# Performance work log

Measured on AMD Instinct MI355X. Metric: run time of the kernel, lower is better.

The kernel has to match this reference:

```python
import jax, jax.numpy as jnp
import numpy as np

N_HEADS = 8
D_HEAD = 64
SCALE = D_HEAD ** -0.5


def setup_inputs() -> dict:
    key = jax.random.key(0)
    k1, k2, k3 = jax.random.split(key, 3)
    B, H, W, C = 16, 32, 32, 512
    ft = jax.random.normal(k1, (B, H, W, C), dtype=jnp.float32)
    # Dense layers: to_qkv -> n_heads*n_dim_heads*3 = 1536 units, to_out -> n_channels
    w_qkv = jax.random.normal(k2, (C, N_HEADS * D_HEAD * 3), dtype=jnp.float32) * (C ** -0.5)
    b_qkv = jnp.zeros((N_HEADS * D_HEAD * 3,), dtype=jnp.float32)
    w_out = jax.random.normal(k3, (N_HEADS * D_HEAD, C), dtype=jnp.float32) * ((N_HEADS * D_HEAD) ** -0.5)
    b_out = jnp.zeros((C,), dtype=jnp.float32)
    return {"ft": ft, "w_qkv": w_qkv, "b_qkv": b_qkv, "w_out": w_out, "b_out": b_out}


def reference(ft, w_qkv, b_qkv, w_out, b_out):
    B, H, W, C = ft.shape
    N = H * W
    x = ft.reshape(B, N, C)                       # b (h w) c
    qkv = x @ w_qkv + b_qkv                       # b n (heads * 3*d_head)
    qkv = qkv.reshape(B, N, N_HEADS, 3 * D_HEAD)  # 'b x (h d) -> b x h d'
    q, k, v = jnp.split(qkv, 3, axis=-1)          # each: b n heads d_head
    attn = jnp.einsum('bxhd,byhd->bxyh', q, k) * SCALE
    attn = jax.nn.softmax(attn, axis=2)           # softmax over key axis y
    res = jnp.einsum('bxyh,byhd->bxhd', attn, v)  # b x h d
    res = res.reshape(B, N, N_HEADS * D_HEAD)     # 'b x h d -> b x (h d)'
    res = res @ w_out + b_out
    res = res + x                                 # residual with pre-qkv flattened input
    return res.reshape(B, H, W, C)
```

## Files before the change

kernel.cpp:

```cpp
#include <hip/hip_runtime.h>
#include <hip/hip_bf16.h>

using u16 = unsigned short;
using u32 = unsigned int;
typedef __attribute__((ext_vector_type(8))) short short8;
typedef __attribute__((ext_vector_type(4))) float f32x4;

#define MFMA16(A, B, C) __builtin_amdgcn_mfma_f32_16x16x32_bf16((A), (B), (C), 0, 0, 0)

__device__ __forceinline__ u16 f2bf(float f) {
  union { float f; u32 i; } v; v.f = f;
  u32 x = v.i;
  return (u16)((x + 0x7fffu + ((x >> 16) & 1u)) >> 16);
}
__device__ __forceinline__ u32 pkbf(float a, float b) {
  union { __hip_bfloat162 h; u32 u; } v;
  v.h = __float22bfloat162_rn(make_float2(a, b));
  return v.u;
}
__device__ __forceinline__ u32 cvtpk(float a, float b) {
  u32 r;
  asm("v_cvt_pk_bf16_f32 %0, %1, %2" : "=v"(r) : "v"(a), "v"(b));
  return r;
}
__device__ __forceinline__ void gl16(const u16* g, u16* l) {
  __builtin_amdgcn_global_load_lds(
      (const __attribute__((address_space(1))) u32*)g,
      (__attribute__((address_space(3))) u32*)l, 16, 0, 0);
}

__global__ __launch_bounds__(256) void conv_x(const float* __restrict__ X,
                                              u16* __restrict__ Xbf) {
  const int i = (blockIdx.x * 256 + threadIdx.x) * 8;
  float4 a = *(const float4*)(X + i);
  float4 b = *(const float4*)(X + i + 4);
  uint4 o;
  o.x = pkbf(a.x, a.y); o.y = pkbf(a.z, a.w);
  o.z = pkbf(b.x, b.y); o.w = pkbf(b.z, b.w);
  *(uint4*)(Xbf + i) = o;
}

__global__ __launch_bounds__(256) void transpose_w(
    const float* __restrict__ Wq, const float* __restrict__ Wo,
    u16* __restrict__ Wqt, u16* __restrict__ Wot) {
  const int z = blockIdx.z;
  if (z == 1 && blockIdx.x >= 16) return;
  const float* src = z ? Wo : Wq;
  u16* dst = z ? Wot : Wqt;
  const int ncols = z ? 512 : 1536;
  __shared__ float tile[32][33];
  const int t = threadIdx.x;
  const int kt = blockIdx.y * 32, nt = blockIdx.x * 32;
  const int r = t >> 3, c4 = (t & 7) * 4;
  float4 v = *(const float4*)(src + (size_t)(kt + r) * ncols + nt + c4);
  tile[r][c4 + 0] = v.x; tile[r][c4 + 1] = v.y;
  tile[r][c4 + 2] = v.z; tile[r][c4 + 3] = v.w;
  __syncthreads();
  uint2 p = make_uint2(pkbf(tile[c4 + 0][r], tile[c4 + 1][r]),
                       pkbf(tile[c4 + 2][r], tile[c4 + 3][r]));
  *(uint2*)(dst + (size_t)(nt + r) * 512 + kt + c4) = p;
}

__global__ __launch_bounds__(512) void qkv_gemm(
    const u16* __restrict__ Xbf, const u16* __restrict__ Wt,
    const float* __restrict__ Bias,
    u16* __restrict__ Qp, u16* __restrict__ Kp, u16* __restrict__ Vt) {
  __shared__ u16 Xs[2][128][32];
  __shared__ u16 Ws[2][256][32];
  const int t = threadIdx.x;
  const int bm = blockIdx.y * 128, bn = blockIdx.x * 256;
  const int w = t >> 6, lane = t & 63, quad = lane >> 4, l16 = lane & 15;
  const int mtb = (w >> 2) * 64, ntb = (w & 3) * 64;
  const int rr = lane >> 2;
  const int gch = ((lane & 3) ^ ((lane >> 3) & 3)) * 8;
  const int sw = (quad ^ ((l16 >> 1) & 3)) * 8;

  const u16* xg0 = Xbf + (size_t)(bm + w * 16 + rr) * 512 + gch;
  const u16* wg0 = Wt + (size_t)(bn + w * 16 + rr) * 512 + gch;
  const u16* wg1 = wg0 + (size_t)128 * 512;
  u16* xl[2] = {&Xs[0][w * 16][0], &Xs[1][w * 16][0]};
  u16* wl[2] = {&Ws[0][w * 16][0], &Ws[1][w * 16][0]};

  f32x4 acc[4][4];
  const f32x4 z4 = {0.f, 0.f, 0.f, 0.f};
  #pragma unroll
  for (int mi = 0; mi < 4; mi++)
    #pragma unroll
    for (int ni = 0; ni < 4; ni++) acc[mi][ni] = z4;

  gl16(xg0, xl[0]);
  gl16(wg0, wl[0]); gl16(wg1, wl[0] + 4096);
  __syncthreads();

  for (int k0 = 0; k0 < 512; k0 += 32) {
    const int cur = (k0 >> 5) & 1;
    if (k0 < 480) {
      const int nxt = cur ^ 1, kn = k0 + 32;
      gl16(xg0 + kn, xl[nxt]);
      gl16(wg0 + kn, wl[nxt]); gl16(wg1 + kn, wl[nxt] + 4096);
    }
    short8 af[4], bf4[4];
    #pragma unroll
    for (int mi = 0; mi < 4; mi++)
      af[mi] = *(const short8*)&Xs[cur][mtb + mi * 16 + l16][sw];
    #pragma unroll
    for (int ni = 0; ni < 4; ni++)
      bf4[ni] = *(const short8*)&Ws[cur][ntb + ni * 16 + l16][sw];
    #pragma unroll
    for (int mi = 0; mi < 4; mi++)
      #pragma unroll
      for (int ni = 0; ni < 4; ni++)
        acc[mi][ni] = MFMA16(af[mi], bf4[ni], acc[mi][ni]);
    __syncthreads();
  }

  #pragma unroll
  for (int ni = 0; ni < 4; ni++) {
    const int g = bn + ntb + ni * 16;
    const int h = g / 192, rm = g % 192;
    const int type = rm >> 6, dbase = rm & 63;
    const float bias = Bias[g + l16];
    const float qsc = (type == 0) ? 0.125f * 1.44269504088896340736f : 1.0f;
    #pragma unroll
    for (int mi = 0; mi < 4; mi++) {
      const int row0 = bm + mtb + mi * 16 + quad * 4;
      const int b = row0 >> 10, n0 = row0 & 1023;
      const size_t bh = (size_t)(b * 8 + h) * 65536;
      if (type == 2) {
        uint2 p = make_uint2(pkbf(acc[mi][ni][0] + bias, acc[mi][ni][1] + bias),
                             pkbf(acc[mi][ni][2] + bias, acc[mi][ni][3] + bias));
        *(uint2*)(Vt + bh + (size_t)(dbase + l16) * 1024 + n0) = p;
      } else {
        u16* dst = (type ? Kp : Qp) + bh;
        #pragma unroll
        for (int r = 0; r < 4; r++)
          dst[(size_t)(n0 + r) * 64 + dbase + l16] =
              f2bf((acc[mi][ni][r] + bias) * qsc);
      }
    }
  }
}

__global__ __launch_bounds__(512, 8) void attn_mfma(
    const u16* __restrict__ Qp, const u16* __restrict__ Kp,
    const u16* __restrict__ Vt, u16* __restrict__ ATT) {
  __shared__ u16 Ks[2][64][64];
  __shared__ u16 Vs[2][64][64];
  const int t = threadIdx.x, w = t >> 6, lane = t & 63;
  const int quad = lane >> 4, l16 = lane & 15;
  const int bx = blockIdx.x;
  const int c = bx & 7, g = bx >> 3;
  const int qt = g & 7, u = g >> 3;
  const int bh_id = u * 8 + c;
  const int b = bh_id >> 3, h = bh_id & 7;
  const size_t bh = (size_t)bh_id * 65536;
  const u16* Qb = Qp + bh;
  const u16* Kb = Kp + bh;
  const u16* Vb = Vt + bh;
  const int q0 = qt * 128 + w * 16;

  const u16* kg = Kb + (size_t)(t >> 3) * 64 + ((t & 7) ^ ((t >> 3) & 7)) * 8;
  const u16* vg = Vb + (size_t)(t >> 3) * 1024 + ((t & 7) ^ ((t >> 3) & 7)) * 8;
  u16* ks0 = &Ks[0][0][0] + w * 512;
  u16* ks1 = &Ks[1][0][0] + w * 512;
  u16* vs0 = &Vs[0][0][0] + w * 512;
  u16* vs1 = &Vs[1][0][0] + w * 512;

  const int m7 = l16 & 7;
  const char* ksb = (const char*)&Ks[0][0][0];
  const char* vsb = (const char*)&Vs[0][0][0];
  const int kb0 = l16 * 128 + (quad ^ m7) * 16;
  const int kb1 = kb0 ^ 64;
  int vo[2];
  #pragma unroll
  for (int ks = 0; ks < 2; ks++)
    vo[ks] = l16 * 128 + ((4 * ks + quad) ^ m7) * 16;

  short8 qf[2];
  #pragma unroll
  for (int ks = 0; ks < 2; ks++)
    qf[ks] = *(const short8*)(Qb + (size_t)(q0 + l16) * 64 + ks * 32 + quad * 8);

  float l_ = 0.f;
  f32x4 Of[4];
  const f32x4 z4 = {0.f, 0.f, 0.f, 0.f};
  #pragma unroll
  for (int ni = 0; ni < 4; ni++) Of[ni] = z4;

  gl16(kg, ks0);
  gl16(vg, vs0);
  __syncthreads();

  for (int kt = 0; kt < 16; ++kt) {
    const int cur = kt & 1;
    if (kt < 15) {
      gl16(kg + (kt + 1) * 4096, cur ? ks0 : ks1);
      gl16(vg + (kt + 1) * 64,   cur ? vs0 : vs1);
    }
    const int co = cur << 13;

    u32 e[4], o[4];
    #pragma unroll
    for (int nt = 0; nt < 4; nt++) {
      short8 k0f = *(const short8*)(ksb + co + kb0 + nt * 2048);
      short8 k1f = *(const short8*)(ksb + co + kb1 + nt * 2048);
      f32x4 s = z4;
      s = MFMA16(k0f, qf[0], s);
      s = MFMA16(k1f, qf[1], s);
      float p0 = __builtin_amdgcn_exp2f(s[0]);
      float p1 = __builtin_amdgcn_exp2f(s[1]);
      float p2 = __builtin_amdgcn_exp2f(s[2]);
      float p3 = __builtin_amdgcn_exp2f(s[3]);
      l_ += (p0 + p1) + (p2 + p3);
      const u32 lo = cvtpk(p0, p1), hi = cvtpk(p2, p3);
      if (nt & 1) { o[(nt >> 1) * 2] = lo; o[(nt >> 1) * 2 + 1] = hi; }
      else        { e[(nt >> 1) * 2] = lo; e[(nt >> 1) * 2 + 1] = hi; }
    }
    #pragma unroll
    for (int i = 0; i < 4; i++) {
      auto t01 = __builtin_amdgcn_permlane32_swap(e[i], o[i], false, false);
      auto xy  = __builtin_amdgcn_permlane16_swap(t01[0], t01[1], false, false);
      e[i] = xy[0]; o[i] = xy[1];
    }
    #pragma unroll
    for (int ks = 0; ks < 2; ks++) {
      union { short8 v; u32 u[4]; } pa;
      pa.u[0] = e[2 * ks]; pa.u[1] = e[2 * ks + 1];
      pa.u[2] = o[2 * ks]; pa.u[3] = o[2 * ks + 1];
      #pragma unroll
      for (int ni = 0; ni < 4; ni++) {
        short8 vf = *(const short8*)(vsb + co + vo[ks] + ni * 2048);
        Of[ni] = MFMA16(pa.v, vf, Of[ni]);
      }
    }
    __syncthreads();
  }
  l_ += __shfl_xor(l_, 16);
  l_ += __shfl_xor(l_, 32);
  float lv[4];
  #pragma unroll
  for (int r = 0; r < 4; r++) lv[r] = __shfl(l_, quad * 4 + r);
  #pragma unroll
  for (int r = 0; r < 4; r++) {
    const float inv = 1.0f / lv[r];
    const int row = b * 1024 + q0 + quad * 4 + r;
    #pragma unroll
    for (int ni = 0; ni < 4; ni++)
      ATT[(size_t)row * 512 + h * 64 + ni * 16 + l16] = f2bf(Of[ni][r] * inv);
  }
}

__global__ __launch_bounds__(256) void out_proj(
    const u16* __restrict__ A, const u16* __restrict__ Wt,
    const float* __restrict__ Bias, const float* __restrict__ FT,
    float* __restrict__ OUT) {
  __shared__ u16 As[2][128][32];
  __shared__ u16 Ws[2][128][32];
  const int t = threadIdx.x;
  const int bm = blockIdx.y * 128, bn = blockIdx.x * 128;
  const int w = t >> 6, lane = t & 63, quad = lane >> 4, l16 = lane & 15;
  const int mtb = (w >> 1) * 64, ntb = (w & 1) * 64;
  const int rr = lane >> 2;
  const int gch = ((lane & 3) ^ ((lane >> 3) & 3)) * 8;
  const int sw = (quad ^ ((l16 >> 1) & 3)) * 8;

  const u16* ag0 = A + (size_t)(bm + w * 16 + rr) * 512 + gch;
  const u16* ag1 = ag0 + (size_t)64 * 512;
  const u16* wg0 = Wt + (size_t)(bn + w * 16 + rr) * 512 + gch;
  const u16* wg1 = wg0 + (size_t)64 * 512;
  u16* al0[2] = {&As[0][w * 16][0], &As[1][w * 16][0]};
  u16* wl0[2] = {&Ws[0][w * 16][0], &Ws[1][w * 16][0]};

  f32x4 acc[4][4];
  const f32x4 z4 = {0.f, 0.f, 0.f, 0.f};
  #pragma unroll
  for (int mi = 0; mi < 4; mi++)
    #pragma unroll
    for (int ni = 0; ni < 4; ni++) acc[mi][ni] = z4;

  gl16(ag0, al0[0]); gl16(ag1, al0[0] + 2048);
  gl16(wg0, wl0[0]); gl16(wg1, wl0[0] + 2048);
  __syncthreads();

  for (int k0 = 0; k0 < 512; k0 += 32) {
    const int cur = (k0 >> 5) & 1;
    if (k0 < 480) {
      const int nxt = cur ^ 1, kn = k0 + 32;
      gl16(ag0 + kn, al0[nxt]); gl16(ag1 + kn, al0[nxt] + 2048);
      gl16(wg0 + kn, wl0[nxt]); gl16(wg1 + kn, wl0[nxt] + 2048);
    }
    short8 af[4], bf4[4];
    #pragma unroll
    for (int mi = 0; mi < 4; mi++)
      af[mi] = *(const short8*)&As[cur][mtb + mi * 16 + l16][sw];
    #pragma unroll
    for (int ni = 0; ni < 4; ni++)
      bf4[ni] = *(const short8*)&Ws[cur][ntb + ni * 16 + l16][sw];
    #pragma unroll
    for (int mi = 0; mi < 4; mi++)
      #pragma unroll
      for (int ni = 0; ni < 4; ni++)
        acc[mi][ni] = MFMA16(af[mi], bf4[ni], acc[mi][ni]);
    __syncthreads();
  }

  #pragma unroll
  for (int ni = 0; ni < 4; ni++) {
    const int g = bn + ntb + ni * 16;
    const float bias = Bias[g + l16];
    #pragma unroll
    for (int mi = 0; mi < 4; mi++) {
      const int row0 = bm + mtb + mi * 16 + quad * 4;
      #pragma unroll
      for (int r = 0; r < 4; r++) {
        const size_t idx = (size_t)(row0 + r) * 512 + g + l16;
        OUT[idx] = acc[mi][ni][r] + bias + FT[idx];
      }
    }
  }
}

extern "C" void kernel_launch(void* const* d_in, const int* in_sizes, int n_in,
                              void* d_out, int out_size, void* d_ws, size_t ws_size,
                              hipStream_t stream) {
  const float* ft    = (const float*)d_in[0];
  const float* w_qkv = (const float*)d_in[1];
  const float* b_qkv = (const float*)d_in[2];
  const float* w_out = (const float*)d_in[3];
  const float* b_out = (const float*)d_in[4];
  float* out = (float*)d_out;

  char* p = (char*)d_ws;
  u16* Xbf    = (u16*)(p);
  u16* ATT    = Xbf;
  u16* Wqkv_t = (u16*)(p + 16777216);
  u16* Wout_t = (u16*)(p + 18350080);
  u16* Qp     = (u16*)(p + 18874368);
  u16* Kp     = (u16*)(p + 35651584);
  u16* Vt     = (u16*)(p + 52428800);

  conv_x     <<<4096, 256, 0, stream>>>(ft, Xbf);
  transpose_w<<<dim3(48, 16, 2), 256, 0, stream>>>(w_qkv, w_out, Wqkv_t, Wout_t);
  qkv_gemm   <<<dim3(6, 128), 512, 0, stream>>>(Xbf, Wqkv_t, b_qkv, Qp, Kp, Vt);
  attn_mfma  <<<dim3(1024), 512, 0, stream>>>(Qp, Kp, Vt, ATT);
  out_proj   <<<dim3(4, 128), 256, 0, stream>>>(ATT, Wout_t, b_out, ft, out);
}
```

Measured before the change: 208.4 us.

## Triple-buffer GEMM LDS stages with partial vmcnt waits and remap block order

New measurement: 195.8 us. 6.0% less time.

```diff
diff --git a/kernel.cpp b/kernel.cpp
--- a/kernel.cpp
+++ b/kernel.cpp
@@ -65,10 +65,12 @@
     const u16* __restrict__ Xbf, const u16* __restrict__ Wt,
     const float* __restrict__ Bias,
     u16* __restrict__ Qp, u16* __restrict__ Kp, u16* __restrict__ Vt) {
-  __shared__ u16 Xs[2][128][32];
-  __shared__ u16 Ws[2][256][32];
+  __shared__ u16 Xs[3][128][32];
+  __shared__ u16 Ws[3][256][32];
   const int t = threadIdx.x;
-  const int bm = blockIdx.y * 128, bn = blockIdx.x * 256;
+  const int lid = blockIdx.y * 6 + blockIdx.x;
+  const int sid = (lid & 7) * 96 + (lid >> 3);
+  const int bm = (sid / 6) * 128, bn = (sid % 6) * 256;
   const int w = t >> 6, lane = t & 63, quad = lane >> 4, l16 = lane & 15;
   const int mtb = (w >> 2) * 64, ntb = (w & 3) * 64;
   const int rr = lane >> 2;
@@ -78,8 +80,6 @@
   const u16* xg0 = Xbf + (size_t)(bm + w * 16 + rr) * 512 + gch;
   const u16* wg0 = Wt + (size_t)(bn + w * 16 + rr) * 512 + gch;
   const u16* wg1 = wg0 + (size_t)128 * 512;
-  u16* xl[2] = {&Xs[0][w * 16][0], &Xs[1][w * 16][0]};
-  u16* wl[2] = {&Ws[0][w * 16][0], &Ws[1][w * 16][0]};
 
   f32x4 acc[4][4];
   const f32x4 z4 = {0.f, 0.f, 0.f, 0.f};
@@ -88,16 +88,21 @@
     #pragma unroll
     for (int ni = 0; ni < 4; ni++) acc[mi][ni] = z4;
 
-  gl16(xg0, xl[0]);
-  gl16(wg0, wl[0]); gl16(wg1, wl[0] + 4096);
-  __syncthreads();
-
-  for (int k0 = 0; k0 < 512; k0 += 32) {
-    const int cur = (k0 >> 5) & 1;
-    if (k0 < 480) {
-      const int nxt = cur ^ 1, kn = k0 + 32;
-      gl16(xg0 + kn, xl[nxt]);
-      gl16(wg0 + kn, wl[nxt]); gl16(wg1 + kn, wl[nxt] + 4096);
+  gl16(xg0, &Xs[0][w * 16][0]);
+  gl16(wg0, &Ws[0][w * 16][0]); gl16(wg1, &Ws[0][w * 16][0] + 4096);
+  gl16(xg0 + 32, &Xs[1][w * 16][0]);
+  gl16(wg0 + 32, &Ws[1][w * 16][0]); gl16(wg1 + 32, &Ws[1][w * 16][0] + 4096);
+  asm volatile("s_waitcnt vmcnt(3)" ::: "memory");
+  __builtin_amdgcn_s_barrier();
+
+  for (int k = 0; k < 16; ++k) {
+    const int cur = k % 3;
+    if (k < 14) {
+      const int nx2 = (k + 2) % 3;
+      const int kn = (k + 2) * 32;
+      gl16(xg0 + kn, &Xs[nx2][w * 16][0]);
+      gl16(wg0 + kn, &Ws[nx2][w * 16][0]);
+      gl16(wg1 + kn, &Ws[nx2][w * 16][0] + 4096);
     }
     short8 af[4], bf4[4];
     #pragma unroll
@@ -111,7 +116,11 @@
       #pragma unroll
       for (int ni = 0; ni < 4; ni++)
         acc[mi][ni] = MFMA16(af[mi], bf4[ni], acc[mi][ni]);
-    __syncthreads();
+    if (k < 15) {
+      if (k < 14) asm volatile("s_waitcnt vmcnt(3) lgkmcnt(0)" ::: "memory");
+      else        asm volatile("s_waitcnt vmcnt(0) lgkmcnt(0)" ::: "memory");
+      __builtin_amdgcn_s_barrier();
+    }
   }
 
   #pragma unroll
@@ -254,10 +263,12 @@
     const u16* __restrict__ A, const u16* __restrict__ Wt,
     const float* __restrict__ Bias, const float* __restrict__ FT,
     float* __restrict__ OUT) {
-  __shared__ u16 As[2][128][32];
-  __shared__ u16 Ws[2][128][32];
+  __shared__ u16 As[3][128][32];
+  __shared__ u16 Ws[3][128][32];
   const int t = threadIdx.x;
-  const int bm = blockIdx.y * 128, bn = blockIdx.x * 128;
+  const int lid = blockIdx.y * 4 + blockIdx.x;
+  const int sid = (lid & 7) * 64 + (lid >> 3);
+  const int bm = (sid / 4) * 128, bn = (sid % 4) * 128;
   const int w = t >> 6, lane = t & 63, quad = lane >> 4, l16 = lane & 15;
   const int mtb = (w >> 1) * 64, ntb = (w & 1) * 64;
   const int rr = lane >> 2;
@@ -268,8 +279,6 @@
   const u16* ag1 = ag0 + (size_t)64 * 512;
   const u16* wg0 = Wt + (size_t)(bn + w * 16 + rr) * 512 + gch;
   const u16* wg1 = wg0 + (size_t)64 * 512;
-  u16* al0[2] = {&As[0][w * 16][0], &As[1][w * 16][0]};
-  u16* wl0[2] = {&Ws[0][w * 16][0], &Ws[1][w * 16][0]};
 
   f32x4 acc[4][4];
   const f32x4 z4 = {0.f, 0.f, 0.f, 0.f};
@@ -278,16 +287,22 @@
     #pragma unroll
     for (int ni = 0; ni < 4; ni++) acc[mi][ni] = z4;
 
-  gl16(ag0, al0[0]); gl16(ag1, al0[0] + 2048);
-  gl16(wg0, wl0[0]); gl16(wg1, wl0[0] + 2048);
-  __syncthreads();
-
-  for (int k0 = 0; k0 < 512; k0 += 32) {
-    const int cur = (k0 >> 5) & 1;
-    if (k0 < 480) {
-      const int nxt = cur ^ 1, kn = k0 + 32;
-      gl16(ag0 + kn, al0[nxt]); gl16(ag1 + kn, al0[nxt] + 2048);
-      gl16(wg0 + kn, wl0[nxt]); gl16(wg1 + kn, wl0[nxt] + 2048);
+  gl16(ag0, &As[0][w * 16][0]); gl16(ag1, &As[0][w * 16][0] + 2048);
+  gl16(wg0, &Ws[0][w * 16][0]); gl16(wg1, &Ws[0][w * 16][0] + 2048);
+  gl16(ag0 + 32, &As[1][w * 16][0]); gl16(ag1 + 32, &As[1][w * 16][0] + 2048);
+  gl16(wg0 + 32, &Ws[1][w * 16][0]); gl16(wg1 + 32, &Ws[1][w * 16][0] + 2048);
+  asm volatile("s_waitcnt vmcnt(4)" ::: "memory");
+  __builtin_amdgcn_s_barrier();
+
+  for (int k = 0; k < 16; ++k) {
+    const int cur = k % 3;
+    if (k < 14) {
+      const int nx2 = (k + 2) % 3;
+      const int kn = (k + 2) * 32;
+      gl16(ag0 + kn, &As[nx2][w * 16][0]);
+      gl16(ag1 + kn, &As[nx2][w * 16][0] + 2048);
+      gl16(wg0 + kn, &Ws[nx2][w * 16][0]);
+      gl16(wg1 + kn, &Ws[nx2][w * 16][0] + 2048);
     }
     short8 af[4], bf4[4];
     #pragma unroll
@@ -301,7 +316,11 @@
       #pragma unroll
       for (int ni = 0; ni < 4; ni++)
         acc[mi][ni] = MFMA16(af[mi], bf4[ni], acc[mi][ni]);
-    __syncthreads();
+    if (k < 15) {
+      if (k < 14) asm volatile("s_waitcnt vmcnt(4) lgkmcnt(0)" ::: "memory");
+      else        asm volatile("s_waitcnt vmcnt(0) lgkmcnt(0)" ::: "memory");
+      __builtin_amdgcn_s_barrier();
+    }
   }
 
   #pragma unroll
```
